# Kernel tuning notes

Measured on AMD Instinct MI355X. Metric: run time of the kernel, lower is better.

Reference implementation:

```python
import jax, jax.numpy as jnp
import numpy as np

T, B, H = 2048, 32, 512

def setup_inputs() -> dict:
    key = jax.random.key(0)
    k1, k2, k3, k4 = jax.random.split(key, 4)
    hidden = jax.random.normal(k1, (1, B, H), dtype=jnp.float32)
    encoder_outputs = jax.random.normal(k2, (T, B, H), dtype=jnp.float32)
    # nn.Linear(2H, H): weight (H, 2H), bias (H,)
    bound = 1.0 / np.sqrt(2 * H)
    W_attn = jax.random.uniform(k3, (H, 2 * H), dtype=jnp.float32, minval=-bound, maxval=bound)
    b_attn = jax.random.uniform(jax.random.fold_in(k3, 1), (H,), dtype=jnp.float32, minval=-bound, maxval=bound)
    stdv = 1.0 / np.sqrt(H)
    v = jax.random.normal(k4, (H,), dtype=jnp.float32) * stdv
    return {"hidden": hidden, "encoder_outputs": encoder_outputs,
            "W_attn": W_attn, "b_attn": b_attn, "v": v}

def reference(hidden, encoder_outputs, W_attn, b_attn, v):
    # hidden: (1,B,H) -> broadcast to (B,T,H); enc: (T,B,H) -> (B,T,H)
    enc = jnp.transpose(encoder_outputs, (1, 0, 2))          # (B,T,H)
    h = jnp.broadcast_to(hidden[0][:, None, :], enc.shape)   # (B,T,H)
    cat = jnp.concatenate([h, enc], axis=2)                  # (B,T,2H)
    energy = jnp.tanh(jnp.einsum('bth,oh->bto', cat, W_attn) + b_attn)  # (B,T,H)
    scores = jnp.einsum('bth,h->bt', energy, v)              # (B,T)
    return jax.nn.softmax(scores, axis=1)[:, None, :]        # (B,1,T)
```

## Files before the change

kernel.cpp:

```cpp
#include <hip/hip_runtime.h>
#include <hip/hip_bf16.h>


#define TT 2048
#define BB 32
#define HH 512

typedef __attribute__((ext_vector_type(8))) short bf16x8;
typedef __attribute__((ext_vector_type(4))) float f32x4;

static __device__ __forceinline__ unsigned cvt2(float a, float b) {
    union { __hip_bfloat162 h; unsigned u; } cv;
    cv.h = __float22bfloat162_rn(make_float2(a, b));
    return cv.u;
}

static __device__ __forceinline__ unsigned short f2bf(float f) {
    unsigned int u = __float_as_uint(f);
    unsigned int r = (u + 0x7FFFu + ((u >> 16) & 1u)) >> 16;
    return (unsigned short)r;
}

static __device__ __forceinline__ float fast_tanh(float x) {
    float e = __expf(2.0f * x);
    return 1.0f - 2.0f * __builtin_amdgcn_rcpf(1.0f + e);
}

static __device__ __forceinline__ void gload_lds16(const void* g, void* l) {
    __builtin_amdgcn_global_load_lds(
        (const __attribute__((address_space(1))) unsigned int*)g,
        (__attribute__((address_space(3))) unsigned int*)l, 16, 0, 0);
}

__global__ void prep_kernel(const float* __restrict__ W,
                            const float* __restrict__ hidden,
                            const float* __restrict__ b_attn,
                            short* __restrict__ W2p,
                            float* __restrict__ hb) {
    __shared__ float hrow[512];
    const int bid = blockIdx.x;
    if (bid < 1024) {
        int idx = bid * 256 + threadIdx.x;
        int nt = idx >> 16;
        int ks = (idx >> 13) & 7;
        int s  = idx & 8191;
        int j  = s >> 6;
        int c  = s & 63;
        int kk = c ^ ((j & 7) << 3);
        int o  = nt * 128 + j;
        int k  = ks * 64 + kk;
        W2p[idx] = (short)f2bf(W[o * 1024 + 512 + k]);
    } else {
        const int hbid = bid - 1024;
        int b = hbid >> 1;
        int o = ((hbid & 1) << 8) + threadIdx.x;
        for (int h = threadIdx.x; h < 512; h += 256) hrow[h] = hidden[b * 512 + h];
        __syncthreads();
        const float4* wr = reinterpret_cast<const float4*>(W + (size_t)o * 1024);
        const float4* hr = reinterpret_cast<const float4*>(hrow);
        float acc = b_attn[o];
#pragma unroll 8
        for (int i = 0; i < 128; ++i) {
            float4 w = wr[i], h4 = hr[i];
            acc += w.x * h4.x + w.y * h4.y + w.z * h4.z + w.w * h4.w;
        }
        hb[b * 512 + o] = acc;
    }
}

__global__ __launch_bounds__(256, 2) void attn_main_kernel(
    const float* __restrict__ enc, const short* __restrict__ W2p,
    const float* __restrict__ hb, const float* __restrict__ v,
    float* __restrict__ scores_part)
{
    __shared__ short As[2][128 * 64];
    __shared__ short Bs[2][128 * 64];
    __shared__ float s_red[2][128];

    const int tid = threadIdx.x;
    const int bid = blockIdx.x;
    const int w = (bid & 7) * 256 + (bid >> 3);
    const int nt = w & 3;
    const int mtile = w >> 2;
    const int b = mtile >> 4;
    const int t0 = (mtile & 15) * 128;

    const int wave = tid >> 6;
    const int lane = tid & 63;
    const int wr = wave >> 1;
    const int wc = wave & 1;
    const int lcol = lane & 15;
    const int lq = lane >> 4;

    const int arow = tid >> 3;
    const int afc = (tid & 7) * 8;
    const float* encbase = enc + ((size_t)(t0 + arow) * BB + b) * HH + afc;
    const short* bsrc = W2p + nt * 65536 + (wave * 4) * 512 + lane * 8;

    f32x4 acc[4][4];
#pragma unroll
    for (int mt = 0; mt < 4; ++mt)
#pragma unroll
        for (int ns = 0; ns < 4; ++ns) acc[mt][ns] = (f32x4){0.f, 0.f, 0.f, 0.f};

    float4 rA0[8], rA1[8];

#define A_LOAD(RA, KS)                                                              \
    {                                                                               \
        _Pragma("unroll")                                                           \
        for (int p = 0; p < 4; ++p) {                                               \
            const float* src = encbase + (size_t)p * 32 * BB * HH + (KS) * 64;      \
            RA[p * 2]     = *reinterpret_cast<const float4*>(src);                  \
            RA[p * 2 + 1] = *reinterpret_cast<const float4*>(src + 4);              \
        }                                                                           \
    }

#define B_STAGE(KS, BUF)                                                            \
    {                                                                               \
        const short* s0 = bsrc + (KS) * 8192;                                       \
        _Pragma("unroll")                                                           \
        for (int c = 0; c < 4; ++c)                                                 \
            gload_lds16(s0 + c * 512, &Bs[BUF][(wave * 4 + c) * 512]);              \
    }

#define A_WRITE(RA, BUF)                                                            \
    {                                                                               \
        _Pragma("unroll")                                                           \
        for (int p = 0; p < 4; ++p) {                                               \
            const int r = p * 32 + arow;                                            \
            uint4 pk;                                                               \
            pk.x = cvt2(RA[p * 2].x, RA[p * 2].y);                                  \
            pk.y = cvt2(RA[p * 2].z, RA[p * 2].w);                                  \
            pk.z = cvt2(RA[p * 2 + 1].x, RA[p * 2 + 1].y);                          \
            pk.w = cvt2(RA[p * 2 + 1].z, RA[p * 2 + 1].w);                          \
            const int cs = afc ^ ((r & 7) << 3);                                    \
            *reinterpret_cast<uint4*>(&As[BUF][r * 64 + cs]) = pk;                  \
        }                                                                           \
    }

#define COMPUTE(BUF)                                                                \
    {                                                                               \
        _Pragma("unroll")                                                           \
        for (int ksub = 0; ksub < 2; ++ksub) {                                      \
            const int kk = ksub * 32 + lq * 8;                                      \
            bf16x8 af[4], bfr[4];                                                   \
            _Pragma("unroll")                                                       \
            for (int mt = 0; mt < 4; ++mt) {                                        \
                const int r = wr * 64 + mt * 16 + lcol;                             \
                af[mt] = *reinterpret_cast<const bf16x8*>(                          \
                    &As[BUF][r * 64 + (kk ^ ((r & 7) << 3))]);                      \
            }                                                                       \
            _Pragma("unroll")                                                       \
            for (int ns = 0; ns < 4; ++ns) {                                        \
                const int j = wc * 64 + ns * 16 + lcol;                             \
                bfr[ns] = *reinterpret_cast<const bf16x8*>(                         \
                    &Bs[BUF][j * 64 + (kk ^ ((j & 7) << 3))]);                      \
            }                                                                       \
            _Pragma("unroll")                                                       \
            for (int mt = 0; mt < 4; ++mt)                                          \
                _Pragma("unroll")                                                   \
                for (int ns = 0; ns < 4; ++ns)                                      \
                    acc[mt][ns] = __builtin_amdgcn_mfma_f32_16x16x32_bf16(          \
                        af[mt], bfr[ns], acc[mt][ns], 0, 0, 0);                     \
        }                                                                           \
    }

    A_LOAD(rA0, 0);
    A_LOAD(rA1, 1);
    B_STAGE(0, 0);
    A_WRITE(rA0, 0);
    __syncthreads();

#pragma unroll
    for (int s2 = 0; s2 < 4; ++s2) {
        const int s = s2 * 2;
        if (s + 2 < 8) A_LOAD(rA0, s + 2);
        B_STAGE(s + 1, 1);
        COMPUTE(0);
        A_WRITE(rA1, 1);
        __syncthreads();
        if (s + 3 < 8) A_LOAD(rA1, s + 3);
        if (s + 2 < 8) B_STAGE(s + 2, 0);
        COMPUTE(1);
        if (s + 2 < 8) {
            A_WRITE(rA0, 0);
            __syncthreads();
        }
    }

    float part[4][4];
#pragma unroll
    for (int mt = 0; mt < 4; ++mt)
#pragma unroll
        for (int j = 0; j < 4; ++j) part[mt][j] = 0.0f;

#pragma unroll
    for (int ns = 0; ns < 4; ++ns) {
        const int o = nt * 128 + wc * 64 + ns * 16 + lcol;
        const float hbv = hb[b * 512 + o];
        const float vv = v[o];
#pragma unroll
        for (int mt = 0; mt < 4; ++mt)
#pragma unroll
            for (int j = 0; j < 4; ++j)
                part[mt][j] = fmaf(fast_tanh(acc[mt][ns][j] + hbv), vv, part[mt][j]);
    }

#pragma unroll
    for (int off = 1; off < 16; off <<= 1)
#pragma unroll
        for (int mt = 0; mt < 4; ++mt)
#pragma unroll
            for (int j = 0; j < 4; ++j)
                part[mt][j] += __shfl_xor(part[mt][j], off, 64);

    if (lcol == 0) {
#pragma unroll
        for (int mt = 0; mt < 4; ++mt)
#pragma unroll
            for (int j = 0; j < 4; ++j)
                s_red[wc][wr * 64 + mt * 16 + lq * 4 + j] = part[mt][j];
    }
    __syncthreads();

    if (tid < 128)
        scores_part[((size_t)nt * BB + b) * TT + t0 + tid] =
            s_red[0][tid] + s_red[1][tid];
}

__global__ void softmax_kernel(const float* __restrict__ sp, float* __restrict__ out) {
    __shared__ float wred[4];
    __shared__ float wsum[4];
    const int b = blockIdx.x;
    const int tid = threadIdx.x;
    float vals[8];
    float mx = -1e30f;
#pragma unroll
    for (int i = 0; i < 8; ++i) {
        const int t = i * 256 + tid;
        const float s = sp[(size_t)b * TT + t] + sp[((size_t)BB + b) * TT + t] +
                        sp[((size_t)2 * BB + b) * TT + t] + sp[((size_t)3 * BB + b) * TT + t];
        vals[i] = s;
        mx = fmaxf(mx, s);
    }
#pragma unroll
    for (int off = 32; off; off >>= 1) mx = fmaxf(mx, __shfl_xor(mx, off, 64));
    if ((tid & 63) == 0) wred[tid >> 6] = mx;
    __syncthreads();
    mx = fmaxf(fmaxf(wred[0], wred[1]), fmaxf(wred[2], wred[3]));
    float s = 0.0f;
#pragma unroll
    for (int i = 0; i < 8; ++i) {
        vals[i] = __expf(vals[i] - mx);
        s += vals[i];
    }
#pragma unroll
    for (int off = 32; off; off >>= 1) s += __shfl_xor(s, off, 64);
    if ((tid & 63) == 0) wsum[tid >> 6] = s;
    __syncthreads();
    s = wsum[0] + wsum[1] + wsum[2] + wsum[3];
    const float inv = 1.0f / s;
#pragma unroll
    for (int i = 0; i < 8; ++i) out[b * TT + i * 256 + tid] = vals[i] * inv;
}

extern "C" void kernel_launch(void* const* d_in, const int* in_sizes, int n_in,
                              void* d_out, int out_size, void* d_ws, size_t ws_size,
                              hipStream_t stream) {
    const float* hidden = (const float*)d_in[0];
    const float* enc    = (const float*)d_in[1];
    const float* W      = (const float*)d_in[2];
    const float* b_attn = (const float*)d_in[3];
    const float* v      = (const float*)d_in[4];
    float* out = (float*)d_out;

    char* base = (char*)d_ws;
    short* W2p = (short*)base;
    float* hb  = (float*)(base + 524288);
    float* sp  = (float*)(base + 589824);

    prep_kernel<<<1088, 256, 0, stream>>>(W, hidden, b_attn, W2p, hb);
    attn_main_kernel<<<2048, 256, 0, stream>>>(enc, W2p, hb, v, sp);
    softmax_kernel<<<32, 256, 0, stream>>>(sp, out);
}
```

Measured before the change: 79.91 us.

## Pre-convert encoder outputs to swizzled bf16 image and stage via direct LDS loads

Adds a prep pass that converts the fp32 encoder outputs into a bf16 tile image already swizzled in the LDS layout. The main GEMM kernel then stages both operands with global_load_lds, with no register round-trip or per-tile conversion, and a simpler double-buffered loop. The cost is an extra full read of the fp32 encoder data plus a 64 MB bf16 write and re-read, and it needs a large workspace; if the workspace is too small it falls back to the old path.

```diff
diff --git a/kernel.cpp b/kernel.cpp
--- a/kernel.cpp
+++ b/kernel.cpp
@@ -30,6 +30,62 @@
     __builtin_amdgcn_global_load_lds(
         (const __attribute__((address_space(1))) unsigned int*)g,
         (__attribute__((address_space(3))) unsigned int*)l, 16, 0, 0);
+}
+
+__global__ void prep_all_kernel(const float* __restrict__ W,
+                                const float* __restrict__ hidden,
+                                const float* __restrict__ b_attn,
+                                const float* __restrict__ enc,
+                                short* __restrict__ W2p,
+                                float* __restrict__ hb,
+                                short* __restrict__ Aimg) {
+    __shared__ float hrow[512];
+    const int bid = blockIdx.x;
+    const int tid = threadIdx.x;
+    if (bid < 16384) {
+        const int gw = bid * 4 + (tid >> 6);
+        const int lane = tid & 63;
+        const int mtile = gw >> 7, r = gw & 127;
+        const int b = mtile >> 4;
+        const int t = (mtile & 15) * 128 + r;
+        const int ks = lane >> 3, blk = lane & 7;
+        const float* src = enc + ((size_t)t * BB + b) * HH + lane * 8;
+        const float4 lo = *reinterpret_cast<const float4*>(src);
+        const float4 hi = *reinterpret_cast<const float4*>(src + 4);
+        uint4 pk;
+        pk.x = cvt2(lo.x, lo.y);
+        pk.y = cvt2(lo.z, lo.w);
+        pk.z = cvt2(hi.x, hi.y);
+        pk.w = cvt2(hi.z, hi.w);
+        short* dst = Aimg + (size_t)mtile * 65536 + ks * 8192 + r * 64 +
+                     ((blk ^ (r & 7)) * 8);
+        *reinterpret_cast<uint4*>(dst) = pk;
+    } else if (bid < 17408) {
+        int idx = (bid - 16384) * 256 + tid;
+        int nt = idx >> 16;
+        int ks = (idx >> 13) & 7;
+        int s  = idx & 8191;
+        int j  = s >> 6;
+        int c  = s & 63;
+        int o  = nt * 128 + j;
+        int k  = ks * 64 + (c ^ ((j & 7) << 3));
+        W2p[idx] = (short)f2bf(W[o * 1024 + 512 + k]);
+    } else {
+        const int hbid = bid - 17408;
+        int b = hbid >> 1;
+        int o = ((hbid & 1) << 8) + tid;
+        for (int h = tid; h < 512; h += 256) hrow[h] = hidden[b * 512 + h];
+        __syncthreads();
+        const float4* wr = reinterpret_cast<const float4*>(W + (size_t)o * 1024);
+        const float4* hr = reinterpret_cast<const float4*>(hrow);
+        float acc = b_attn[o];
+#pragma unroll 8
+        for (int i = 0; i < 128; ++i) {
+            float4 w = wr[i], h4 = hr[i];
+            acc += w.x * h4.x + w.y * h4.y + w.z * h4.z + w.w * h4.w;
+        }
+        hb[b * 512 + o] = acc;
+    }
 }
 
 __global__ void prep_kernel(const float* __restrict__ W,
@@ -46,9 +102,8 @@
         int s  = idx & 8191;
         int j  = s >> 6;
         int c  = s & 63;
-        int kk = c ^ ((j & 7) << 3);
         int o  = nt * 128 + j;
-        int k  = ks * 64 + kk;
+        int k  = ks * 64 + (c ^ ((j & 7) << 3));
         W2p[idx] = (short)f2bf(W[o * 1024 + 512 + k]);
     } else {
         const int hbid = bid - 1024;
@@ -67,76 +122,6 @@
         hb[b * 512 + o] = acc;
     }
 }
-
-__global__ __launch_bounds__(256, 2) void attn_main_kernel(
-    const float* __restrict__ enc, const short* __restrict__ W2p,
-    const float* __restrict__ hb, const float* __restrict__ v,
-    float* __restrict__ scores_part)
-{
-    __shared__ short As[2][128 * 64];
-    __shared__ short Bs[2][128 * 64];
-    __shared__ float s_red[2][128];
-
-    const int tid = threadIdx.x;
-    const int bid = blockIdx.x;
-    const int w = (bid & 7) * 256 + (bid >> 3);
-    const int nt = w & 3;
-    const int mtile = w >> 2;
-    const int b = mtile >> 4;
-    const int t0 = (mtile & 15) * 128;
-
-    const int wave = tid >> 6;
-    const int lane = tid & 63;
-    const int wr = wave >> 1;
-    const int wc = wave & 1;
-    const int lcol = lane & 15;
-    const int lq = lane >> 4;
-
-    const int arow = tid >> 3;
-    const int afc = (tid & 7) * 8;
-    const float* encbase = enc + ((size_t)(t0 + arow) * BB + b) * HH + afc;
-    const short* bsrc = W2p + nt * 65536 + (wave * 4) * 512 + lane * 8;
-
-    f32x4 acc[4][4];
-#pragma unroll
-    for (int mt = 0; mt < 4; ++mt)
-#pragma unroll
-        for (int ns = 0; ns < 4; ++ns) acc[mt][ns] = (f32x4){0.f, 0.f, 0.f, 0.f};
-
-    float4 rA0[8], rA1[8];
-
-#define A_LOAD(RA, KS)                                                              \
-    {                                                                               \
-        _Pragma("unroll")                                                           \
-        for (int p = 0; p < 4; ++p) {                                               \
-            const float* src = encbase + (size_t)p * 32 * BB * HH + (KS) * 64;      \
-            RA[p * 2]     = *reinterpret_cast<const float4*>(src);                  \
-            RA[p * 2 + 1] = *reinterpret_cast<const float4*>(src + 4);              \
-        }                                                                           \
-    }
-
-#define B_STAGE(KS, BUF)                                                            \
-    {                                                                               \
-        const short* s0 = bsrc + (KS) * 8192;                                       \
-        _Pragma("unroll")                                                           \
-        for (int c = 0; c < 4; ++c)                                                 \
-            gload_lds16(s0 + c * 512, &Bs[BUF][(wave * 4 + c) * 512]);              \
-    }
-
-#define A_WRITE(RA, BUF)                                                            \
-    {                                                                               \
-        _Pragma("unroll")                                                           \
-        for (int p = 0; p < 4; ++p) {                                               \
-            const int r = p * 32 + arow;                                            \
-            uint4 pk;                                                               \
-            pk.x = cvt2(RA[p * 2].x, RA[p * 2].y);                                  \
-            pk.y = cvt2(RA[p * 2].z, RA[p * 2].w);                                  \
-            pk.z = cvt2(RA[p * 2 + 1].x, RA[p * 2 + 1].y);                          \
-            pk.w = cvt2(RA[p * 2 + 1].z, RA[p * 2 + 1].w);                          \
-            const int cs = afc ^ ((r & 7) << 3);                                    \
-            *reinterpret_cast<uint4*>(&As[BUF][r * 64 + cs]) = pk;                  \
-        }                                                                           \
-    }
 
 #define COMPUTE(BUF)                                                                \
     {                                                                               \
@@ -165,25 +150,189 @@
         }                                                                           \
     }
 
-    A_LOAD(rA0, 0);
-    A_LOAD(rA1, 1);
-    B_STAGE(0, 0);
-    A_WRITE(rA0, 0);
+__global__ __launch_bounds__(256, 2) void attn_main_lds_kernel(
+    const short* __restrict__ Aimg, const short* __restrict__ W2p,
+    const float* __restrict__ hb, const float* __restrict__ v,
+    float* __restrict__ scores_part)
+{
+    __shared__ short As[2][128 * 64];
+    __shared__ short Bs[2][128 * 64];
+    __shared__ float s_red[2][128];
+
+    const int tid = threadIdx.x;
+    const int bid = blockIdx.x;
+    const int w = (bid & 7) * 256 + (bid >> 3);
+    const int nt = w & 3;
+    const int mtile = w >> 2;
+    const int b = mtile >> 4;
+    const int t0 = (mtile & 15) * 128;
+
+    const int wave = tid >> 6;
+    const int lane = tid & 63;
+    const int wr = wave >> 1;
+    const int wc = wave & 1;
+    const int lcol = lane & 15;
+    const int lq = lane >> 4;
+
+    const short* asrc = Aimg + (size_t)mtile * 65536 + wave * 2048 + lane * 8;
+    const short* bsrc = W2p + (size_t)nt * 65536 + wave * 2048 + lane * 8;
+
+    f32x4 acc[4][4];
+#pragma unroll
+    for (int mt = 0; mt < 4; ++mt)
+#pragma unroll
+        for (int ns = 0; ns < 4; ++ns) acc[mt][ns] = (f32x4){0.f, 0.f, 0.f, 0.f};
+
+#define AB_STAGE(KS, BUF)                                                           \
+    {                                                                               \
+        const short* a0 = asrc + (KS) * 8192;                                       \
+        const short* b0 = bsrc + (KS) * 8192;                                       \
+        _Pragma("unroll")                                                           \
+        for (int c = 0; c < 4; ++c) {                                               \
+            gload_lds16(a0 + c * 512, &As[BUF][wave * 2048 + c * 512]);             \
+            gload_lds16(b0 + c * 512, &Bs[BUF][wave * 2048 + c * 512]);             \
+        }                                                                           \
+    }
+
+    AB_STAGE(0, 0);
+    __syncthreads();
+
+#pragma unroll
+    for (int s = 0; s < 8; ++s) {
+        if (s < 7) AB_STAGE(s + 1, (s & 1) ^ 1);
+        COMPUTE(s & 1);
+        __syncthreads();
+    }
+
+    float part[4][4];
+#pragma unroll
+    for (int mt = 0; mt < 4; ++mt)
+#pragma unroll
+        for (int j = 0; j < 4; ++j) part[mt][j] = 0.0f;
+
+#pragma unroll
+    for (int ns = 0; ns < 4; ++ns) {
+        const int o = nt * 128 + wc * 64 + ns * 16 + lcol;
+        const float hbv = hb[b * 512 + o];
+        const float vv = v[o];
+#pragma unroll
+        for (int mt = 0; mt < 4; ++mt)
+#pragma unroll
+            for (int j = 0; j < 4; ++j)
+                part[mt][j] = fmaf(fast_tanh(acc[mt][ns][j] + hbv), vv, part[mt][j]);
+    }
+
+#pragma unroll
+    for (int off = 1; off < 16; off <<= 1)
+#pragma unroll
+        for (int mt = 0; mt < 4; ++mt)
+#pragma unroll
+            for (int j = 0; j < 4; ++j)
+                part[mt][j] += __shfl_xor(part[mt][j], off, 64);
+
+    if (lcol == 0) {
+#pragma unroll
+        for (int mt = 0; mt < 4; ++mt)
+#pragma unroll
+            for (int j = 0; j < 4; ++j)
+                s_red[wc][wr * 64 + mt * 16 + lq * 4 + j] = part[mt][j];
+    }
+    __syncthreads();
+
+    if (tid < 128)
+        scores_part[((size_t)nt * BB + b) * TT + t0 + tid] =
+            s_red[0][tid] + s_red[1][tid];
+}
+
+__global__ __launch_bounds__(256, 2) void attn_main_kernel(
+    const float* __restrict__ enc, const short* __restrict__ W2p,
+    const float* __restrict__ hb, const float* __restrict__ v,
+    float* __restrict__ scores_part)
+{
+    __shared__ short As[2][128 * 64];
+    __shared__ short Bs[2][128 * 64];
+    __shared__ float s_red[2][128];
+
+    const int tid = threadIdx.x;
+    const int bid = blockIdx.x;
+    const int w = (bid & 7) * 256 + (bid >> 3);
+    const int nt = w & 3;
+    const int mtile = w >> 2;
+    const int b = mtile >> 4;
+    const int t0 = (mtile & 15) * 128;
+
+    const int wave = tid >> 6;
+    const int lane = tid & 63;
+    const int wr = wave >> 1;
+    const int wc = wave & 1;
+    const int lcol = lane & 15;
+    const int lq = lane >> 4;
+
+    const int arow = tid >> 3;
+    const int afc = (tid & 7) * 8;
+    const float* encbase = enc + ((size_t)(t0 + arow) * BB + b) * HH + afc;
+    const short* bsrc = W2p + nt * 65536 + (wave * 4) * 512 + lane * 8;
+
+    f32x4 acc[4][4];
+#pragma unroll
+    for (int mt = 0; mt < 4; ++mt)
+#pragma unroll
+        for (int ns = 0; ns < 4; ++ns) acc[mt][ns] = (f32x4){0.f, 0.f, 0.f, 0.f};
+
+    float4 rA0[8], rA1[8];
+
+#define F_A_LOAD(RA, KS)                                                            \
+    {                                                                               \
+        _Pragma("unroll")                                                           \
+        for (int p = 0; p < 4; ++p) {                                               \
+            const float* src = encbase + (size_t)p * 32 * BB * HH + (KS) * 64;      \
+            RA[p * 2]     = *reinterpret_cast<const float4*>(src);                  \
+            RA[p * 2 + 1] = *reinterpret_cast<const float4*>(src + 4);              \
+        }                                                                           \
+    }
+
+#define F_B_STAGE(KS, BUF)                                                          \
+    {                                                                               \
+        const short* s0 = bsrc + (KS) * 8192;                                       \
+        _Pragma("unroll")                                                           \
+        for (int c = 0; c < 4; ++c)                                                 \
+            gload_lds16(s0 + c * 512, &Bs[BUF][(wave * 4 + c) * 512]);              \
+    }
+
+#define F_A_WRITE(RA, BUF)                                                          \
+    {                                                                               \
+        _Pragma("unroll")                                                           \
+        for (int p = 0; p < 4; ++p) {                                               \
+            const int r = p * 32 + arow;                                            \
+            uint4 pk;                                                               \
+            pk.x = cvt2(RA[p * 2].x, RA[p * 2].y);                                  \
+            pk.y = cvt2(RA[p * 2].z, RA[p * 2].w);                                  \
+            pk.z = cvt2(RA[p * 2 + 1].x, RA[p * 2 + 1].y);                          \
+            pk.w = cvt2(RA[p * 2 + 1].z, RA[p * 2 + 1].w);                          \
+            const int cs = afc ^ ((r & 7) << 3);                                    \
+            *reinterpret_cast<uint4*>(&As[BUF][r * 64 + cs]) = pk;                  \
+        }                                                                           \
+    }
+
+    F_A_LOAD(rA0, 0);
+    F_A_LOAD(rA1, 1);
+    F_B_STAGE(0, 0);
+    F_A_WRITE(rA0, 0);
     __syncthreads();
 
 #pragma unroll
     for (int s2 = 0; s2 < 4; ++s2) {
         const int s = s2 * 2;
-        if (s + 2 < 8) A_LOAD(rA0, s + 2);
-        B_STAGE(s + 1, 1);
+        if (s + 2 < 8) F_A_LOAD(rA0, s + 2);
+        F_B_STAGE(s + 1, 1);
         COMPUTE(0);
-        A_WRITE(rA1, 1);
+        F_A_WRITE(rA1, 1);
         __syncthreads();
-        if (s + 3 < 8) A_LOAD(rA1, s + 3);
-        if (s + 2 < 8) B_STAGE(s + 2, 0);
+        if (s + 3 < 8) F_A_LOAD(rA1, s + 3);
+        if (s + 2 < 8) F_B_STAGE(s + 2, 0);
         COMPUTE(1);
         if (s + 2 < 8) {
-            A_WRITE(rA0, 0);
+            F_A_WRITE(rA0, 0);
             __syncthreads();
         }
     }
@@ -278,8 +427,15 @@
     short* W2p = (short*)base;
     float* hb  = (float*)(base + 524288);
     float* sp  = (float*)(base + 589824);
-
-    prep_kernel<<<1088, 256, 0, stream>>>(W, hidden, b_attn, W2p, hb);
-    attn_main_kernel<<<2048, 256, 0, stream>>>(enc, W2p, hb, v, sp);
+    short* Aimg = (short*)(base + 1638400);
+    const size_t need = 1638400ull + 67108864ull;
+
+    if (ws_size >= need) {
+        prep_all_kernel<<<17472, 256, 0, stream>>>(W, hidden, b_attn, enc, W2p, hb, Aimg);
+        attn_main_lds_kernel<<<2048, 256, 0, stream>>>(Aimg, W2p, hb, v, sp);
+    } else {
+        prep_kernel<<<1088, 256, 0, stream>>>(W, hidden, b_attn, W2p, hb);
+        attn_main_kernel<<<2048, 256, 0, stream>>>(enc, W2p, hb, v, sp);
+    }
     softmax_kernel<<<32, 256, 0, stream>>>(sp, out);
 }
```

Result: slower. 114.2 us (+42.9%).

## Tile main GEMM over contiguous encoder rows instead of per-batch strided rows

Applied to the files above, without the earlier changes.

The main kernel now treats the encoder tensor as a flat (T*B, H) matrix, with each M-tile covering 128 consecutive rows rather than 128 time steps of one batch. Encoder loads become contiguous instead of strided by B*H. In exchange, the hidden-bias lookup varies per row, so it needs per-element gathers from hb. The softmax kernel now reads partial scores with a stride of B, which is less coalesced.

```diff
diff --git a/kernel.cpp b/kernel.cpp
--- a/kernel.cpp
+++ b/kernel.cpp
@@ -46,9 +46,8 @@
         int s  = idx & 8191;
         int j  = s >> 6;
         int c  = s & 63;
-        int kk = c ^ ((j & 7) << 3);
         int o  = nt * 128 + j;
-        int k  = ks * 64 + kk;
+        int k  = ks * 64 + (c ^ ((j & 7) << 3));
         W2p[idx] = (short)f2bf(W[o * 1024 + 512 + k]);
     } else {
         const int hbid = bid - 1024;
@@ -82,8 +81,7 @@
     const int w = (bid & 7) * 256 + (bid >> 3);
     const int nt = w & 3;
     const int mtile = w >> 2;
-    const int b = mtile >> 4;
-    const int t0 = (mtile & 15) * 128;
+    const int r0 = mtile * 128;
 
     const int wave = tid >> 6;
     const int lane = tid & 63;
@@ -94,7 +92,7 @@
 
     const int arow = tid >> 3;
     const int afc = (tid & 7) * 8;
-    const float* encbase = enc + ((size_t)(t0 + arow) * BB + b) * HH + afc;
+    const float* encbase = enc + (size_t)(r0 + arow) * HH + afc;
     const short* bsrc = W2p + nt * 65536 + (wave * 4) * 512 + lane * 8;
 
     f32x4 acc[4][4];
@@ -109,7 +107,7 @@
     {                                                                               \
         _Pragma("unroll")                                                           \
         for (int p = 0; p < 4; ++p) {                                               \
-            const float* src = encbase + (size_t)p * 32 * BB * HH + (KS) * 64;      \
+            const float* src = encbase + (size_t)p * 32 * HH + (KS) * 64;           \
             RA[p * 2]     = *reinterpret_cast<const float4*>(src);                  \
             RA[p * 2 + 1] = *reinterpret_cast<const float4*>(src + 4);              \
         }                                                                           \
@@ -197,13 +195,18 @@
 #pragma unroll
     for (int ns = 0; ns < 4; ++ns) {
         const int o = nt * 128 + wc * 64 + ns * 16 + lcol;
-        const float hbv = hb[b * 512 + o];
         const float vv = v[o];
-#pragma unroll
-        for (int mt = 0; mt < 4; ++mt)
-#pragma unroll
-            for (int j = 0; j < 4; ++j)
-                part[mt][j] = fmaf(fast_tanh(acc[mt][ns][j] + hbv), vv, part[mt][j]);
+        const float* hbcol = hb + o;
+#pragma unroll
+        for (int mt = 0; mt < 4; ++mt) {
+            const int bbase = (mt * 16 + lq * 4) & 31;
+#pragma unroll
+            for (int j = 0; j < 4; ++j) {
+                const float hbv = hbcol[(bbase + j) * 512];
+                const float x = acc[mt][ns][j] + hbv;
+                part[mt][j] = fmaf(fast_tanh(x), vv, part[mt][j]);
+            }
+        }
     }
 
 #pragma unroll
@@ -224,7 +227,7 @@
     __syncthreads();
 
     if (tid < 128)
-        scores_part[((size_t)nt * BB + b) * TT + t0 + tid] =
+        scores_part[(size_t)nt * (TT * BB) + r0 + tid] =
             s_red[0][tid] + s_red[1][tid];
 }
 
@@ -238,8 +241,9 @@
 #pragma unroll
     for (int i = 0; i < 8; ++i) {
         const int t = i * 256 + tid;
-        const float s = sp[(size_t)b * TT + t] + sp[((size_t)BB + b) * TT + t] +
-                        sp[((size_t)2 * BB + b) * TT + t] + sp[((size_t)3 * BB + b) * TT + t];
+        const size_t r = (size_t)t * BB + b;
+        const float s = sp[r] + sp[(size_t)(TT * BB) + r] +
+                        sp[(size_t)2 * (TT * BB) + r] + sp[(size_t)3 * (TT * BB) + r];
         vals[i] = s;
         mx = fmaxf(mx, s);
     }
```

Measured after the change: 87.15 us. 9.1% more time.
